# Performance work log

Measured on AMD Instinct MI355X. Metric: run time of the kernel, lower is better.

## Reference

```python
import jax, jax.numpy as jnp
import numpy as np

N, DIM_V, DIM_MM, DIM_O = 1024, 2048, 64, 2048
EPS_LOG = 1e-3


def setup_inputs() -> dict:
    key = jax.random.key(0)
    ks = jax.random.split(key, 12)
    feature_visual = jax.random.normal(ks[0], (N, DIM_V), dtype=jnp.float32)
    # valid boxes (x1, y1, x2, y2) inside an ~800x600 image
    x1 = jax.random.uniform(ks[1], (N, 1)) * 700.0
    y1 = jax.random.uniform(ks[2], (N, 1)) * 500.0
    w = jax.random.uniform(ks[3], (N, 1)) * 180.0 + 16.0
    h = jax.random.uniform(ks[4], (N, 1)) * 180.0 + 16.0
    rois = jnp.concatenate([x1, y1, x1 + w, y1 + h], axis=1)
    s = 0.02
    return {
        "feature_visual": feature_visual,
        "rois": rois,
        "Wk": jax.random.normal(ks[5], (DIM_V, DIM_MM), dtype=jnp.float32) * s,
        "bk": jnp.zeros((DIM_MM,), jnp.float32),
        "Wq": jax.random.normal(ks[6], (DIM_V, DIM_MM), dtype=jnp.float32) * s,
        "bq": jnp.zeros((DIM_MM,), jnp.float32),
        "Wv": jax.random.normal(ks[7], (DIM_V, DIM_O), dtype=jnp.float32) * s,
        "bv": jnp.zeros((DIM_O,), jnp.float32),
        "G1": jax.random.normal(ks[8], (4, DIM_MM), dtype=jnp.float32) * s,
        "g1": jnp.zeros((DIM_MM,), jnp.float32),
        "G2": jax.random.normal(ks[9], (DIM_MM, 1), dtype=jnp.float32) * s,
        "g2": jnp.zeros((1,), jnp.float32),
    }


def _geometry_weight(rois, G1, g1, G2, g2):
    # pairwise relative geometry features [N, N, 4], then MLP -> ReLU scalar weight [N, N]
    wh = rois[:, 2:4] - rois[:, 0:2]                      # [N, 2] box width/height
    ctr = 0.5 * (rois[:, 0:2] + rois[:, 2:4])             # [N, 2] centers
    d = ctr[None, :, :] - ctr[:, None, :]                 # [N, N, 2] (j relative to i)
    f12 = jnp.log(jnp.abs(d) / wh[:, None, :] + EPS_LOG)  # log(|dx|/wi), log(|dy|/hi)
    f34 = jnp.log(wh[None, :, :] / wh[:, None, :])        # log(wj/wi), log(hj/hi)
    geo = jnp.concatenate([f12, f34], axis=-1)            # [N, N, 4]
    h = jax.nn.relu(jnp.einsum('ijf,fm->ijm', geo, G1) + g1)
    w = jax.nn.relu(jnp.einsum('ijm,mo->ijo', h, G2) + g2)
    return w[..., 0]                                      # [N, N]


def reference(feature_visual, rois, Wk, bk, Wq, bq, Wv, bv, G1, g1, G2, g2):
    fv = jax.nn.relu(feature_visual)                      # pre-activation features
    k = fv @ Wk + bk                                      # [N, dim_mm]
    q = fv @ Wq + bq                                      # [N, dim_mm]
    v = fv @ Wv + bv                                      # [N, dim_o]
    scale = 1.0 / np.sqrt(DIM_MM).astype(np.float32)
    visual_weight = (q @ k.T) * scale                     # [N, N]: score[i,j] = <q_i... wait
    # torch: (query.unsqueeze(0) * key.unsqueeze(1)).sum(2) -> score[i,j] = <k_i, q_j>
    visual_weight = (k @ q.T) * scale
    geometry_weight = _geometry_weight(rois, G1, g1, G2, g2)
    attention = jnp.exp(visual_weight) * geometry_weight  # [N, N]
    n = attention.shape[0]
    attention = attention * (1.0 - jnp.eye(n, dtype=attention.dtype))  # zero diagonal
    attention = attention / (attention.sum(axis=1, keepdims=True) + 1e-10)
    return attention @ v                                  # [N, dim_o]
```

## Files before the change

kernel.cpp:

```cpp
#include <hip/hip_runtime.h>
#include <hip/hip_bf16.h>

#define NR 1024
#define DV 2048
#define DMM 64
#define DO 2048

typedef __attribute__((ext_vector_type(8))) __bf16 bf16x8;
typedef __attribute__((ext_vector_type(4))) float f32x4;

__device__ __forceinline__ float relu_f(float x) { return fmaxf(x, 0.f); }

__device__ __forceinline__ unsigned short f2bf(float x) {
    union { float f; unsigned int u; } v; v.f = x;
    unsigned int r = v.u + 0x7fffu + ((v.u >> 16) & 1u);
    return (unsigned short)(r >> 16);
}

__device__ __forceinline__ void gload_lds16(const void* g, void* l) {
    __builtin_amdgcn_global_load_lds(
        (const __attribute__((address_space(1))) void*)g,
        (__attribute__((address_space(3))) void*)l, 16, 0, 0);
}

__device__ __forceinline__ void transpose_tile(
    const float* __restrict__ W, unsigned short* __restrict__ Wt,
    int Ncols, int k0, int o0, float (*ld)[65])
{
    const int t = threadIdx.x;
    const int r = t >> 2;
    const int c0 = (t & 3) * 16;
    #pragma unroll
    for (int i = 0; i < 4; ++i) {
        float4 v = *reinterpret_cast<const float4*>(&W[(size_t)(k0 + r) * Ncols + o0 + c0 + i * 4]);
        ld[c0 + i * 4 + 0][r] = v.x;
        ld[c0 + i * 4 + 1][r] = v.y;
        ld[c0 + i * 4 + 2][r] = v.z;
        ld[c0 + i * 4 + 3][r] = v.w;
    }
    __syncthreads();
    const int o = t >> 2;
    const int kc = (t & 3) * 16;
    unsigned int u[8];
    #pragma unroll
    for (int j = 0; j < 8; ++j) {
        float x0 = ld[o][kc + 2 * j], x1 = ld[o][kc + 2 * j + 1];
        u[j] = (unsigned)f2bf(x0) | ((unsigned)f2bf(x1) << 16);
    }
    uint4* dst = reinterpret_cast<uint4*>(&Wt[(size_t)(o0 + o) * DV + k0 + kc]);
    dst[0] = make_uint4(u[0], u[1], u[2], u[3]);
    dst[1] = make_uint4(u[4], u[5], u[6], u[7]);
}

__global__ __launch_bounds__(256) void prep_kernel(
    const float* __restrict__ feat,
    const float* __restrict__ Wk, const float* __restrict__ Wq, const float* __restrict__ Wv,
    const float* __restrict__ rois,
    unsigned short* __restrict__ fvb, unsigned short* __restrict__ WkqT,
    unsigned short* __restrict__ WvT,
    float4* __restrict__ boxf, float2* __restrict__ boxinv)
{
    __shared__ float ld[64][65];
    const int bid = blockIdx.x;
    if (bid < 1024) {
        const int idx = bid * 256 + threadIdx.x;
        const float4 a = *reinterpret_cast<const float4*>(feat + (size_t)idx * 8);
        const float4 b = *reinterpret_cast<const float4*>(feat + (size_t)idx * 8 + 4);
        uint4 o;
        o.x = (unsigned)f2bf(relu_f(a.x)) | ((unsigned)f2bf(relu_f(a.y)) << 16);
        o.y = (unsigned)f2bf(relu_f(a.z)) | ((unsigned)f2bf(relu_f(a.w)) << 16);
        o.z = (unsigned)f2bf(relu_f(b.x)) | ((unsigned)f2bf(relu_f(b.y)) << 16);
        o.w = (unsigned)f2bf(relu_f(b.z)) | ((unsigned)f2bf(relu_f(b.w)) << 16);
        *reinterpret_cast<uint4*>(fvb + (size_t)idx * 8) = o;
    } else if (bid < 2048) {
        const int idx = bid - 1024;
        transpose_tile(Wv, WvT, DO, (idx >> 5) * 64, (idx & 31) * 64, ld);
    } else if (bid < 2080) {
        transpose_tile(Wk, WkqT, DMM, (bid - 2048) * 64, 0, ld);
    } else if (bid < 2112) {
        transpose_tile(Wq, WkqT + 64 * DV, DMM, (bid - 2080) * 64, 0, ld);
    } else {
        const int idx = (bid - 2112) * 256 + threadIdx.x;
        const float4 r = *reinterpret_cast<const float4*>(rois + (size_t)idx * 4);
        const float w = r.z - r.x, h = r.w - r.y;
        boxf[idx]   = make_float4(0.5f * (r.x + r.z), 0.5f * (r.y + r.w), __logf(w), __logf(h));
        boxinv[idx] = make_float2(1.f / w, 1.f / h);
    }
}

template<int NT, int LDA, int LDB>
__device__ __forceinline__ void mfma_tile_pipe(
    const unsigned short* __restrict__ A, const unsigned short* __restrict__ Bt,
    int bm0, int bn0, unsigned short* As, unsigned short* Bs, f32x4 (&acc)[2][4])
{
    const int t = threadIdx.x;
    const int w = t >> 6, lane = t & 63;
    const int wr = w >> 1, wc = w & 1;
    const int fr = lane & 15, fq = lane >> 4;
    const int sr = lane >> 3;
    const int sc = ((lane & 7) ^ sr) * 8;

    const unsigned short* ga0 = A  + (size_t)(bm0 + w * 16 +  0 + sr) * LDA + sc;
    const unsigned short* ga1 = A  + (size_t)(bm0 + w * 16 +  8 + sr) * LDA + sc;
    const unsigned short* gb0 = Bt + (size_t)(bn0 + w * 32 +  0 + sr) * LDB + sc;
    const unsigned short* gb1 = Bt + (size_t)(bn0 + w * 32 +  8 + sr) * LDB + sc;
    const unsigned short* gb2 = Bt + (size_t)(bn0 + w * 32 + 16 + sr) * LDB + sc;
    const unsigned short* gb3 = Bt + (size_t)(bn0 + w * 32 + 24 + sr) * LDB + sc;

#define STAGE(buf, ts_) do {                                                  \
        const size_t ko_ = (size_t)(ts_) * 64;                                \
        gload_lds16(ga0 + ko_, &As[(buf) * 4096 + w * 1024]);                 \
        gload_lds16(ga1 + ko_, &As[(buf) * 4096 + w * 1024 + 512]);           \
        gload_lds16(gb0 + ko_, &Bs[(buf) * 8192 + w * 2048]);                 \
        gload_lds16(gb1 + ko_, &Bs[(buf) * 8192 + w * 2048 + 512]);           \
        gload_lds16(gb2 + ko_, &Bs[(buf) * 8192 + w * 2048 + 1024]);          \
        gload_lds16(gb3 + ko_, &Bs[(buf) * 8192 + w * 2048 + 1536]);          \
    } while (0)

#define COMPUTE(buf) do {                                                                     \
        const int kx_ = fr & 7;                                                               \
        const int clo_ = (fq ^ kx_) * 8, chi_ = ((fq + 4) ^ kx_) * 8;                         \
        bf16x8 afl[2], afh[2], bfl[4], bfh[4];                                                \
        _Pragma("unroll")                                                                     \
        for (int m = 0; m < 2; ++m) {                                                         \
            const int rb = (buf) * 4096 + (wr * 32 + m * 16 + fr) * 64;                       \
            afl[m] = *reinterpret_cast<const bf16x8*>(&As[rb + clo_]);                        \
            afh[m] = *reinterpret_cast<const bf16x8*>(&As[rb + chi_]);                        \
        }                                                                                     \
        _Pragma("unroll")                                                                     \
        for (int n = 0; n < 4; ++n) {                                                         \
            const int cb = (buf) * 8192 + (wc * 64 + n * 16 + fr) * 64;                       \
            bfl[n] = *reinterpret_cast<const bf16x8*>(&Bs[cb + clo_]);                        \
            bfh[n] = *reinterpret_cast<const bf16x8*>(&Bs[cb + chi_]);                        \
        }                                                                                     \
        _Pragma("unroll")                                                                     \
        for (int m = 0; m < 2; ++m)                                                           \
            _Pragma("unroll")                                                                 \
            for (int n = 0; n < 4; ++n) {                                                     \
                acc[m][n] = __builtin_amdgcn_mfma_f32_16x16x32_bf16(afl[m], bfl[n], acc[m][n], 0, 0, 0); \
                acc[m][n] = __builtin_amdgcn_mfma_f32_16x16x32_bf16(afh[m], bfh[n], acc[m][n], 0, 0, 0); \
            }                                                                                 \
    } while (0)

    STAGE(0, 0);
    if (NT > 1) STAGE(1, 1);

    #pragma unroll 2
    for (int ts = 0; ts < NT - 1; ++ts) {
        asm volatile("s_waitcnt vmcnt(6)" ::: "memory");
        asm volatile("s_barrier" ::: "memory");
        COMPUTE(ts & 1);
        asm volatile("s_barrier" ::: "memory");
        if (ts + 2 < NT) STAGE(ts & 1, ts + 2);
    }
    asm volatile("s_waitcnt vmcnt(0)" ::: "memory");
    asm volatile("s_barrier" ::: "memory");
    COMPUTE((NT - 1) & 1);
#undef STAGE
#undef COMPUTE
}

__global__ __launch_bounds__(256) void gemm_vt_kq(
    const unsigned short* __restrict__ WvT, const unsigned short* __restrict__ fvb,
    const unsigned short* __restrict__ WkqT,
    const float* __restrict__ bv, const float* __restrict__ bk, const float* __restrict__ bq,
    unsigned short* __restrict__ vT, unsigned short* __restrict__ kqb)
{
    __shared__ unsigned short As[2 * 64 * 64];
    __shared__ unsigned short Bs[2 * 128 * 64];
    const int bid = blockIdx.x;
    const bool is_kq = bid >= 256;
    const unsigned short* A  = is_kq ? fvb  : WvT;
    const unsigned short* Bt = is_kq ? WkqT : fvb;
    const int bm0 = is_kq ? (bid - 256) * 64 : (bid >> 3) * 64;
    const int bn0 = is_kq ? 0 : (bid & 7) * 128;

    f32x4 acc[2][4] = {};
    mfma_tile_pipe<DV / 64, DV, DV>(A, Bt, bm0, bn0, As, Bs, acc);

    const int t = threadIdx.x;
    const int w = t >> 6, lane = t & 63;
    const int wr = w >> 1, wc = w & 1;
    const int fr = lane & 15, fq = lane >> 4;
    if (!is_kq) {
        #pragma unroll
        for (int m = 0; m < 2; ++m)
            #pragma unroll
            for (int r = 0; r < 4; ++r) {
                const int row = bm0 + wr * 32 + m * 16 + fq * 4 + r;
                const float badd = bv[row];
                #pragma unroll
                for (int n = 0; n < 4; ++n) {
                    const int col = bn0 + wc * 64 + n * 16 + fr;
                    vT[(size_t)row * NR + col] = f2bf(acc[m][n][r] + badd);
                }
            }
    } else {
        #pragma unroll
        for (int m = 0; m < 2; ++m)
            #pragma unroll
            for (int r = 0; r < 4; ++r) {
                const int row = bm0 + wr * 32 + m * 16 + fq * 4 + r;
                #pragma unroll
                for (int n = 0; n < 4; ++n) {
                    const int col = wc * 64 + n * 16 + fr;
                    const float badd = (col < 64) ? bk[col] : bq[col - 64];
                    kqb[(size_t)row * 128 + col] = f2bf(acc[m][n][r] + badd);
                }
            }
    }
}

__global__ __launch_bounds__(256) void gemm_s(
    const unsigned short* __restrict__ kqb, float* __restrict__ S)
{
    __shared__ unsigned short As[2 * 64 * 64];
    __shared__ unsigned short Bs[2 * 128 * 64];
    const int bm0 = blockIdx.y * 64;
    const int bn0 = blockIdx.x * 128;
    f32x4 acc[2][4] = {};
    mfma_tile_pipe<1, 128, 128>(kqb, kqb + 64, bm0, bn0, As, Bs, acc);
    const int t = threadIdx.x;
    const int w = t >> 6, lane = t & 63;
    const int wr = w >> 1, wc = w & 1;
    const int fr = lane & 15, fq = lane >> 4;
    #pragma unroll
    for (int m = 0; m < 2; ++m)
        #pragma unroll
        for (int r = 0; r < 4; ++r) {
            const int row = bm0 + wr * 32 + m * 16 + fq * 4 + r;
            #pragma unroll
            for (int n = 0; n < 4; ++n) {
                const int col = bn0 + wc * 64 + n * 16 + fr;
                S[(size_t)row * NR + col] = acc[m][n][r] * 0.125f;
            }
        }
}

__global__ __launch_bounds__(256) void gemm_out(
    const unsigned short* __restrict__ attb, const unsigned short* __restrict__ vT,
    float* __restrict__ out)
{
    __shared__ unsigned short As[2 * 64 * 64];
    __shared__ unsigned short Bs[2 * 128 * 64];
    const int bm0 = blockIdx.y * 64;
    const int bn0 = blockIdx.x * 128;
    f32x4 acc[2][4] = {};
    mfma_tile_pipe<NR / 64, NR, NR>(attb, vT, bm0, bn0, As, Bs, acc);
    const int t = threadIdx.x;
    const int w = t >> 6, lane = t & 63;
    const int wr = w >> 1, wc = w & 1;
    const int fr = lane & 15, fq = lane >> 4;
    #pragma unroll
    for (int m = 0; m < 2; ++m)
        #pragma unroll
        for (int r = 0; r < 4; ++r) {
            const int row = bm0 + wr * 32 + m * 16 + fq * 4 + r;
            #pragma unroll
            for (int n = 0; n < 4; ++n) {
                const int col = bn0 + wc * 64 + n * 16 + fr;
                out[(size_t)row * DO + col] = acc[m][n][r];
            }
        }
}

#define MLP_STEP(A_, B_, C_, D_, E_, F_)                                            \
    {                                                                               \
        float h_ = fmaf(ff1[ch], A_, fmaf(ff2[ch], B_, fmaf(ff3[ch], C_,            \
                   fmaf(ff4[ch], D_, E_))));                                        \
        h_ = fmaxf(h_, 0.f);                                                        \
        gw[ch] = fmaf(h_, F_, gw[ch]);                                              \
    }

__global__ __launch_bounds__(256) void attn_kernel(
    const float* __restrict__ S,
    const float4* __restrict__ boxf, const float2* __restrict__ boxinv,
    const float* __restrict__ G1, const float* __restrict__ g1,
    const float* __restrict__ G2, const float* __restrict__ g2,
    unsigned short* __restrict__ att)
{
    __shared__ float G1s[4][64];
    __shared__ float g1s[64];
    __shared__ float G2s[64];
    __shared__ float red[4];
    const int i = blockIdx.x;
    const int t = threadIdx.x;
    if (t < 64) {
        G1s[0][t] = G1[t];
        G1s[1][t] = G1[64 + t];
        G1s[2][t] = G1[128 + t];
        G1s[3][t] = G1[192 + t];
        g1s[t] = g1[t];
        G2s[t] = G2[t];
    }
    __syncthreads();
    const float4 bi = boxf[i];
    const float2 ivi = boxinv[i];
    const float g2v = g2[0];

    float ff1[4], ff2[4], ff3[4], ff4[4], sc[4], gw[4] = {0.f, 0.f, 0.f, 0.f};
    #pragma unroll
    for (int ch = 0; ch < 4; ++ch) {
        const int j = ch * 256 + t;
        const float4 bj = boxf[j];
        sc[ch] = S[(size_t)i * NR + j];
        ff1[ch] = __logf(fmaf(fabsf(bj.x - bi.x), ivi.x, 1e-3f));
        ff2[ch] = __logf(fmaf(fabsf(bj.y - bi.y), ivi.y, 1e-3f));
        ff3[ch] = bj.z - bi.z;
        ff4[ch] = bj.w - bi.w;
    }

    for (int mt = 0; mt < 64; mt += 8) {
        const float4 A0 = *reinterpret_cast<const float4*>(&G1s[0][mt]);
        const float4 A1 = *reinterpret_cast<const float4*>(&G1s[0][mt + 4]);
        const float4 B0 = *reinterpret_cast<const float4*>(&G1s[1][mt]);
        const float4 B1 = *reinterpret_cast<const float4*>(&G1s[1][mt + 4]);
        const float4 C0 = *reinterpret_cast<const float4*>(&G1s[2][mt]);
        const float4 C1 = *reinterpret_cast<const float4*>(&G1s[2][mt + 4]);
        const float4 D0 = *reinterpret_cast<const float4*>(&G1s[3][mt]);
        const float4 D1 = *reinterpret_cast<const float4*>(&G1s[3][mt + 4]);
        const float4 E0 = *reinterpret_cast<const float4*>(&g1s[mt]);
        const float4 E1 = *reinterpret_cast<const float4*>(&g1s[mt + 4]);
        const float4 F0 = *reinterpret_cast<const float4*>(&G2s[mt]);
        const float4 F1 = *reinterpret_cast<const float4*>(&G2s[mt + 4]);
        #pragma unroll
        for (int ch = 0; ch < 4; ++ch) {
            MLP_STEP(A0.x, B0.x, C0.x, D0.x, E0.x, F0.x)
            MLP_STEP(A0.y, B0.y, C0.y, D0.y, E0.y, F0.y)
            MLP_STEP(A0.z, B0.z, C0.z, D0.z, E0.z, F0.z)
            MLP_STEP(A0.w, B0.w, C0.w, D0.w, E0.w, F0.w)
            MLP_STEP(A1.x, B1.x, C1.x, D1.x, E1.x, F1.x)
            MLP_STEP(A1.y, B1.y, C1.y, D1.y, E1.y, F1.y)
            MLP_STEP(A1.z, B1.z, C1.z, D1.z, E1.z, F1.z)
            MLP_STEP(A1.w, B1.w, C1.w, D1.w, E1.w, F1.w)
        }
    }

    float vals[4];
    float rsum = 0.f;
    #pragma unroll
    for (int ch = 0; ch < 4; ++ch) {
        const float gwp = fmaxf(gw[ch] + g2v, 0.f);
        float a = __expf(sc[ch]) * gwp;
        if (ch * 256 + t == i) a = 0.f;
        vals[ch] = a;
        rsum += a;
    }
    #pragma unroll
    for (int o = 32; o > 0; o >>= 1) rsum += __shfl_down(rsum, o, 64);
    if ((t & 63) == 0) red[t >> 6] = rsum;
    __syncthreads();
    const float inv = 1.f / (red[0] + red[1] + red[2] + red[3] + 1e-10f);
    #pragma unroll
    for (int ch = 0; ch < 4; ++ch)
        att[(size_t)i * NR + ch * 256 + t] = f2bf(vals[ch] * inv);
}

extern "C" void kernel_launch(void* const* d_in, const int* in_sizes, int n_in,
                              void* d_out, int out_size, void* d_ws, size_t ws_size,
                              hipStream_t stream) {
    const float* feat = (const float*)d_in[0];
    const float* rois = (const float*)d_in[1];
    const float* Wk   = (const float*)d_in[2];
    const float* bk   = (const float*)d_in[3];
    const float* Wq   = (const float*)d_in[4];
    const float* bq   = (const float*)d_in[5];
    const float* Wv   = (const float*)d_in[6];
    const float* bv   = (const float*)d_in[7];
    const float* G1   = (const float*)d_in[8];
    const float* g1   = (const float*)d_in[9];
    const float* G2   = (const float*)d_in[10];
    const float* g2   = (const float*)d_in[11];
    float* out = (float*)d_out;
    char* ws = (char*)d_ws;

    unsigned short* kqb  = (unsigned short*)ws;
    float4* boxf         = (float4*)(ws + (256 << 10));
    float2* boxinv       = (float2*)(ws + (272 << 10));
    unsigned short* fvb  = (unsigned short*)(ws + (512 << 10));
    unsigned short* WvT  = (unsigned short*)(ws + (512 << 10) + (4 << 20));
    unsigned short* WkqT = (unsigned short*)(ws + (512 << 10) + (12 << 20));
    unsigned short* vT   = (unsigned short*)(ws + (1024 << 10) + (12 << 20));
    unsigned short* attb = (unsigned short*)(ws + (1024 << 10) + (16 << 20));
    float* Sbuf          = (float*)(ws + (1024 << 10) + (18 << 20));

    prep_kernel<<<2116, 256, 0, stream>>>(feat, Wk, Wq, Wv, rois, fvb, WkqT, WvT, boxf, boxinv);
    gemm_vt_kq<<<272, 256, 0, stream>>>(WvT, fvb, WkqT, bv, bk, bq, vT, kqb);
    gemm_s<<<dim3(8, 16), 256, 0, stream>>>(kqb, Sbuf);
    attn_kernel<<<NR, 256, 0, stream>>>(Sbuf, boxf, boxinv, G1, g1, G2, g2, attb);
    gemm_out<<<dim3(DO / 128, NR / 64), 256, 0, stream>>>(attb, vT, out);
}
```

Measured before the change: 64.77 us.

## Fuse score GEMM into attention kernel with per-row bf16 dot products

Removes the separate k·qᵀ MFMA GEMM kernel and its fp32 score buffer; each attention block now computes its row of scores directly from the bf16 k/q buffer with scalar FMAs. This avoids one launch and the write and read-back of the N×N score matrix. In exchange the attention kernel does extra ALU work and issues strided 16-byte loads of q rows that depend on L2 reuse.

```diff
diff --git a/kernel.cpp b/kernel.cpp
--- a/kernel.cpp
+++ b/kernel.cpp
@@ -15,6 +15,13 @@
     union { float f; unsigned int u; } v; v.f = x;
     unsigned int r = v.u + 0x7fffu + ((v.u >> 16) & 1u);
     return (unsigned short)(r >> 16);
+}
+
+__device__ __forceinline__ float bflo(unsigned int u) {
+    union { unsigned int x; float f; } v; v.x = u << 16; return v.f;
+}
+__device__ __forceinline__ float bfhi(unsigned int u) {
+    union { unsigned int x; float f; } v; v.x = u & 0xffff0000u; return v.f;
 }
 
 __device__ __forceinline__ void gload_lds16(const void* g, void* l) {
@@ -211,32 +218,6 @@
     }
 }
 
-__global__ __launch_bounds__(256) void gemm_s(
-    const unsigned short* __restrict__ kqb, float* __restrict__ S)
-{
-    __shared__ unsigned short As[2 * 64 * 64];
-    __shared__ unsigned short Bs[2 * 128 * 64];
-    const int bm0 = blockIdx.y * 64;
-    const int bn0 = blockIdx.x * 128;
-    f32x4 acc[2][4] = {};
-    mfma_tile_pipe<1, 128, 128>(kqb, kqb + 64, bm0, bn0, As, Bs, acc);
-    const int t = threadIdx.x;
-    const int w = t >> 6, lane = t & 63;
-    const int wr = w >> 1, wc = w & 1;
-    const int fr = lane & 15, fq = lane >> 4;
-    #pragma unroll
-    for (int m = 0; m < 2; ++m)
-        #pragma unroll
-        for (int r = 0; r < 4; ++r) {
-            const int row = bm0 + wr * 32 + m * 16 + fq * 4 + r;
-            #pragma unroll
-            for (int n = 0; n < 4; ++n) {
-                const int col = bn0 + wc * 64 + n * 16 + fr;
-                S[(size_t)row * NR + col] = acc[m][n][r] * 0.125f;
-            }
-        }
-}
-
 __global__ __launch_bounds__(256) void gemm_out(
     const unsigned short* __restrict__ attb, const unsigned short* __restrict__ vT,
     float* __restrict__ out)
@@ -273,7 +254,7 @@
     }
 
 __global__ __launch_bounds__(256) void attn_kernel(
-    const float* __restrict__ S,
+    const unsigned short* __restrict__ kqb,
     const float4* __restrict__ boxf, const float2* __restrict__ boxinv,
     const float* __restrict__ G1, const float* __restrict__ g1,
     const float* __restrict__ G2, const float* __restrict__ g2,
@@ -282,6 +263,7 @@
     __shared__ float G1s[4][64];
     __shared__ float g1s[64];
     __shared__ float G2s[64];
+    __shared__ float ksf[64];
     __shared__ float red[4];
     const int i = blockIdx.x;
     const int t = threadIdx.x;
@@ -292,18 +274,38 @@
         G1s[3][t] = G1[192 + t];
         g1s[t] = g1[t];
         G2s[t] = G2[t];
+        ksf[t] = bflo((unsigned int)kqb[(size_t)i * 128 + t]);
     }
     __syncthreads();
     const float4 bi = boxf[i];
     const float2 ivi = boxinv[i];
     const float g2v = g2[0];
 
+    float dot[4] = {0.f, 0.f, 0.f, 0.f};
+    #pragma unroll
+    for (int c4 = 0; c4 < 8; ++c4) {
+        const float4 k0 = *reinterpret_cast<const float4*>(&ksf[c4 * 8]);
+        const float4 k1 = *reinterpret_cast<const float4*>(&ksf[c4 * 8 + 4]);
+        #pragma unroll
+        for (int ch = 0; ch < 4; ++ch) {
+            const int j = ch * 256 + t;
+            const uint4 qv = *reinterpret_cast<const uint4*>(
+                &kqb[(size_t)j * 128 + 64 + c4 * 8]);
+            float d = dot[ch];
+            d = fmaf(k0.x, bflo(qv.x), d); d = fmaf(k0.y, bfhi(qv.x), d);
+            d = fmaf(k0.z, bflo(qv.y), d); d = fmaf(k0.w, bfhi(qv.y), d);
+            d = fmaf(k1.x, bflo(qv.z), d); d = fmaf(k1.y, bfhi(qv.z), d);
+            d = fmaf(k1.z, bflo(qv.w), d); d = fmaf(k1.w, bfhi(qv.w), d);
+            dot[ch] = d;
+        }
+    }
+
     float ff1[4], ff2[4], ff3[4], ff4[4], sc[4], gw[4] = {0.f, 0.f, 0.f, 0.f};
     #pragma unroll
     for (int ch = 0; ch < 4; ++ch) {
         const int j = ch * 256 + t;
         const float4 bj = boxf[j];
-        sc[ch] = S[(size_t)i * NR + j];
+        sc[ch] = dot[ch] * 0.125f;
         ff1[ch] = __logf(fmaf(fabsf(bj.x - bi.x), ivi.x, 1e-3f));
         ff2[ch] = __logf(fmaf(fabsf(bj.y - bi.y), ivi.y, 1e-3f));
         ff3[ch] = bj.z - bi.z;
@@ -382,11 +384,9 @@
     unsigned short* WkqT = (unsigned short*)(ws + (512 << 10) + (12 << 20));
     unsigned short* vT   = (unsigned short*)(ws + (1024 << 10) + (12 << 20));
     unsigned short* attb = (unsigned short*)(ws + (1024 << 10) + (16 << 20));
-    float* Sbuf          = (float*)(ws + (1024 << 10) + (18 << 20));
 
     prep_kernel<<<2116, 256, 0, stream>>>(feat, Wk, Wq, Wv, rois, fvb, WkqT, WvT, boxf, boxinv);
     gemm_vt_kq<<<272, 256, 0, stream>>>(WvT, fvb, WkqT, bv, bk, bq, vT, kqb);
-    gemm_s<<<dim3(8, 16), 256, 0, stream>>>(kqb, Sbuf);
-    attn_kernel<<<NR, 256, 0, stream>>>(Sbuf, boxf, boxinv, G1, g1, G2, g2, attb);
+    attn_kernel<<<NR, 256, 0, stream>>>(kqb, boxf, boxinv, G1, g1, G2, g2, attb);
     gemm_out<<<dim3(DO / 128, NR / 64), 256, 0, stream>>>(attb, vT, out);
 }
```

After: 84.64 us. +30.7%, slower.

## Fuse score GEMM with geometry MLP and defer row normalization into output GEMM

Applied to the files above, without the earlier changes.

Merges the S=k·qᵀ GEMM and the geometry/attention kernel into a single tiled kernel. The geometry MLP now runs directly on the MFMA accumulator fragments, so the fp32 S buffer is no longer written and read back. Row-sum normalization moves into the final attention·V GEMM, which sums the bf16 A tiles while it loads them and scales the output rows. This removes one launch and a 4 MB intermediate round trip. In exchange it adds per-element box loads in the fused kernel and normalizes with sums of bf16-rounded values instead of fp32 values.

```diff
diff --git a/kernel.cpp b/kernel.cpp
--- a/kernel.cpp
+++ b/kernel.cpp
@@ -7,6 +7,7 @@
 #define DO 2048
 
 typedef __attribute__((ext_vector_type(8))) __bf16 bf16x8;
+typedef __attribute__((ext_vector_type(8))) unsigned short u16x8;
 typedef __attribute__((ext_vector_type(4))) float f32x4;
 
 __device__ __forceinline__ float relu_f(float x) { return fmaxf(x, 0.f); }
@@ -15,6 +16,10 @@
     union { float f; unsigned int u; } v; v.f = x;
     unsigned int r = v.u + 0x7fffu + ((v.u >> 16) & 1u);
     return (unsigned short)(r >> 16);
+}
+
+__device__ __forceinline__ float bflo(unsigned int u) {
+    union { unsigned int x; float f; } v; v.x = u << 16; return v.f;
 }
 
 __device__ __forceinline__ void gload_lds16(const void* g, void* l) {
@@ -88,10 +93,11 @@
     }
 }
 
-template<int NT, int LDA, int LDB>
+template<int NT, int LDA, int LDB, int BNR, bool SUMA>
 __device__ __forceinline__ void mfma_tile_pipe(
     const unsigned short* __restrict__ A, const unsigned short* __restrict__ Bt,
-    int bm0, int bn0, unsigned short* As, unsigned short* Bs, f32x4 (&acc)[2][4])
+    int bm0, int bn0, unsigned short* As, unsigned short* Bs,
+    f32x4 (&acc)[2][BNR], float* rs)
 {
     const int t = threadIdx.x;
     const int w = t >> 6, lane = t & 63;
@@ -100,27 +106,27 @@
     const int sr = lane >> 3;
     const int sc = ((lane & 7) ^ sr) * 8;
 
-    const unsigned short* ga0 = A  + (size_t)(bm0 + w * 16 +  0 + sr) * LDA + sc;
-    const unsigned short* ga1 = A  + (size_t)(bm0 + w * 16 +  8 + sr) * LDA + sc;
-    const unsigned short* gb0 = Bt + (size_t)(bn0 + w * 32 +  0 + sr) * LDB + sc;
-    const unsigned short* gb1 = Bt + (size_t)(bn0 + w * 32 +  8 + sr) * LDB + sc;
-    const unsigned short* gb2 = Bt + (size_t)(bn0 + w * 32 + 16 + sr) * LDB + sc;
-    const unsigned short* gb3 = Bt + (size_t)(bn0 + w * 32 + 24 + sr) * LDB + sc;
-
-#define STAGE(buf, ts_) do {                                                  \
-        const size_t ko_ = (size_t)(ts_) * 64;                                \
-        gload_lds16(ga0 + ko_, &As[(buf) * 4096 + w * 1024]);                 \
-        gload_lds16(ga1 + ko_, &As[(buf) * 4096 + w * 1024 + 512]);           \
-        gload_lds16(gb0 + ko_, &Bs[(buf) * 8192 + w * 2048]);                 \
-        gload_lds16(gb1 + ko_, &Bs[(buf) * 8192 + w * 2048 + 512]);           \
-        gload_lds16(gb2 + ko_, &Bs[(buf) * 8192 + w * 2048 + 1024]);          \
-        gload_lds16(gb3 + ko_, &Bs[(buf) * 8192 + w * 2048 + 1536]);          \
+    const unsigned short* ga0 = A + (size_t)(bm0 + w * 16 + 0 + sr) * LDA + sc;
+    const unsigned short* ga1 = A + (size_t)(bm0 + w * 16 + 8 + sr) * LDA + sc;
+    const unsigned short* gb[BNR];
+    #pragma unroll
+    for (int g = 0; g < BNR; ++g)
+        gb[g] = Bt + (size_t)(bn0 + w * (BNR * 8) + g * 8 + sr) * LDB + sc;
+
+#define STAGE(buf, ts_) do {                                                   \
+        const size_t ko_ = (size_t)(ts_) * 64;                                 \
+        gload_lds16(ga0 + ko_, &As[(buf) * 4096 + w * 1024]);                  \
+        gload_lds16(ga1 + ko_, &As[(buf) * 4096 + w * 1024 + 512]);            \
+        _Pragma("unroll")                                                      \
+        for (int g = 0; g < BNR; ++g)                                          \
+            gload_lds16(gb[g] + ko_,                                           \
+                &Bs[(buf) * (BNR * 2048) + w * (BNR * 512) + g * 512]);        \
     } while (0)
 
 #define COMPUTE(buf) do {                                                                     \
         const int kx_ = fr & 7;                                                               \
         const int clo_ = (fq ^ kx_) * 8, chi_ = ((fq + 4) ^ kx_) * 8;                         \
-        bf16x8 afl[2], afh[2], bfl[4], bfh[4];                                                \
+        bf16x8 afl[2], afh[2], bfl[BNR], bfh[BNR];                                            \
         _Pragma("unroll")                                                                     \
         for (int m = 0; m < 2; ++m) {                                                         \
             const int rb = (buf) * 4096 + (wr * 32 + m * 16 + fr) * 64;                       \
@@ -128,15 +134,25 @@
             afh[m] = *reinterpret_cast<const bf16x8*>(&As[rb + chi_]);                        \
         }                                                                                     \
         _Pragma("unroll")                                                                     \
-        for (int n = 0; n < 4; ++n) {                                                         \
-            const int cb = (buf) * 8192 + (wc * 64 + n * 16 + fr) * 64;                       \
+        for (int n = 0; n < BNR; ++n) {                                                       \
+            const int cb = (buf) * (BNR * 2048) + (wc * (BNR * 16) + n * 16 + fr) * 64;       \
             bfl[n] = *reinterpret_cast<const bf16x8*>(&Bs[cb + clo_]);                        \
             bfh[n] = *reinterpret_cast<const bf16x8*>(&Bs[cb + chi_]);                        \
+        }                                                                                     \
+        if (SUMA && wc == 0) {                                                                \
+            _Pragma("unroll")                                                                 \
+            for (int m = 0; m < 2; ++m) {                                                     \
+                u16x8 sl = __builtin_bit_cast(u16x8, afl[m]);                                 \
+                u16x8 sh = __builtin_bit_cast(u16x8, afh[m]);                                 \
+                _Pragma("unroll")                                                             \
+                for (int e = 0; e < 8; ++e)                                                   \
+                    rs[m] += bflo(sl[e]) + bflo(sh[e]);                                       \
+            }                                                                                 \
         }                                                                                     \
         _Pragma("unroll")                                                                     \
         for (int m = 0; m < 2; ++m)                                                           \
             _Pragma("unroll")                                                                 \
-            for (int n = 0; n < 4; ++n) {                                                     \
+            for (int n = 0; n < BNR; ++n) {                                                   \
                 acc[m][n] = __builtin_amdgcn_mfma_f32_16x16x32_bf16(afl[m], bfl[n], acc[m][n], 0, 0, 0); \
                 acc[m][n] = __builtin_amdgcn_mfma_f32_16x16x32_bf16(afh[m], bfh[n], acc[m][n], 0, 0, 0); \
             }                                                                                 \
@@ -147,7 +163,8 @@
 
     #pragma unroll 2
     for (int ts = 0; ts < NT - 1; ++ts) {
-        asm volatile("s_waitcnt vmcnt(6)" ::: "memory");
+        if (BNR == 4) { asm volatile("s_waitcnt vmcnt(6)" ::: "memory"); }
+        else          { asm volatile("s_waitcnt vmcnt(4)" ::: "memory"); }
         asm volatile("s_barrier" ::: "memory");
         COMPUTE(ts & 1);
         asm volatile("s_barrier" ::: "memory");
@@ -176,7 +193,7 @@
     const int bn0 = is_kq ? 0 : (bid & 7) * 128;
 
     f32x4 acc[2][4] = {};
-    mfma_tile_pipe<DV / 64, DV, DV>(A, Bt, bm0, bn0, As, Bs, acc);
+    mfma_tile_pipe<DV / 64, DV, DV, 4, false>(A, Bt, bm0, bn0, As, Bs, acc, nullptr);
 
     const int t = threadIdx.x;
     const int w = t >> 6, lane = t & 63;
@@ -211,79 +228,29 @@
     }
 }
 
-__global__ __launch_bounds__(256) void gemm_s(
-    const unsigned short* __restrict__ kqb, float* __restrict__ S)
-{
-    __shared__ unsigned short As[2 * 64 * 64];
-    __shared__ unsigned short Bs[2 * 128 * 64];
-    const int bm0 = blockIdx.y * 64;
-    const int bn0 = blockIdx.x * 128;
-    f32x4 acc[2][4] = {};
-    mfma_tile_pipe<1, 128, 128>(kqb, kqb + 64, bm0, bn0, As, Bs, acc);
-    const int t = threadIdx.x;
-    const int w = t >> 6, lane = t & 63;
-    const int wr = w >> 1, wc = w & 1;
-    const int fr = lane & 15, fq = lane >> 4;
-    #pragma unroll
-    for (int m = 0; m < 2; ++m)
-        #pragma unroll
-        for (int r = 0; r < 4; ++r) {
-            const int row = bm0 + wr * 32 + m * 16 + fq * 4 + r;
-            #pragma unroll
-            for (int n = 0; n < 4; ++n) {
-                const int col = bn0 + wc * 64 + n * 16 + fr;
-                S[(size_t)row * NR + col] = acc[m][n][r] * 0.125f;
-            }
-        }
-}
-
-__global__ __launch_bounds__(256) void gemm_out(
-    const unsigned short* __restrict__ attb, const unsigned short* __restrict__ vT,
-    float* __restrict__ out)
-{
-    __shared__ unsigned short As[2 * 64 * 64];
-    __shared__ unsigned short Bs[2 * 128 * 64];
-    const int bm0 = blockIdx.y * 64;
-    const int bn0 = blockIdx.x * 128;
-    f32x4 acc[2][4] = {};
-    mfma_tile_pipe<NR / 64, NR, NR>(attb, vT, bm0, bn0, As, Bs, acc);
-    const int t = threadIdx.x;
-    const int w = t >> 6, lane = t & 63;
-    const int wr = w >> 1, wc = w & 1;
-    const int fr = lane & 15, fq = lane >> 4;
-    #pragma unroll
-    for (int m = 0; m < 2; ++m)
-        #pragma unroll
-        for (int r = 0; r < 4; ++r) {
-            const int row = bm0 + wr * 32 + m * 16 + fq * 4 + r;
-            #pragma unroll
-            for (int n = 0; n < 4; ++n) {
-                const int col = bn0 + wc * 64 + n * 16 + fr;
-                out[(size_t)row * DO + col] = acc[m][n][r];
-            }
-        }
-}
-
-#define MLP_STEP(A_, B_, C_, D_, E_, F_)                                            \
+#define MLP_STEP8(A_, B_, C_, D_, E_, F_)                                           \
     {                                                                               \
-        float h_ = fmaf(ff1[ch], A_, fmaf(ff2[ch], B_, fmaf(ff3[ch], C_,            \
-                   fmaf(ff4[ch], D_, E_))));                                        \
-        h_ = fmaxf(h_, 0.f);                                                        \
-        gw[ch] = fmaf(h_, F_, gw[ch]);                                              \
-    }
-
-__global__ __launch_bounds__(256) void attn_kernel(
-    const float* __restrict__ S,
+        _Pragma("unroll")                                                           \
+        for (int p = 0; p < 8; ++p) {                                               \
+            float h_ = fmaf(ff1[p], A_, fmaf(ff2[p], B_, fmaf(ff3[p], C_,           \
+                       fmaf(ff4[p], D_, E_))));                                     \
+            h_ = fmaxf(h_, 0.f);                                                    \
+            gw[p] = fmaf(h_, F_, gw[p]);                                            \
+        }                                                                           \
+    }
+
+__global__ __launch_bounds__(256) void s_geo(
+    const unsigned short* __restrict__ kqb,
     const float4* __restrict__ boxf, const float2* __restrict__ boxinv,
     const float* __restrict__ G1, const float* __restrict__ g1,
     const float* __restrict__ G2, const float* __restrict__ g2,
     unsigned short* __restrict__ att)
 {
+    __shared__ unsigned short As[64 * 64];
+    __shared__ unsigned short Bs[64 * 64];
     __shared__ float G1s[4][64];
     __shared__ float g1s[64];
     __shared__ float G2s[64];
-    __shared__ float red[4];
-    const int i = blockIdx.x;
     const int t = threadIdx.x;
     if (t < 64) {
         G1s[0][t] = G1[t];
@@ -294,66 +261,118 @@
         G2s[t] = G2[t];
     }
     __syncthreads();
-    const float4 bi = boxf[i];
-    const float2 ivi = boxinv[i];
+
+    const int bm0 = blockIdx.y * 64;
+    const int bn0 = blockIdx.x * 64;
+    f32x4 acc[2][2] = {};
+    mfma_tile_pipe<1, 128, 128, 2, false>(kqb, kqb + 64, bm0, bn0, As, Bs, acc, nullptr);
+
+    const int w = t >> 6, lane = t & 63;
+    const int wr = w >> 1, wc = w & 1;
+    const int fr = lane & 15, fq = lane >> 4;
     const float g2v = g2[0];
 
-    float ff1[4], ff2[4], ff3[4], ff4[4], sc[4], gw[4] = {0.f, 0.f, 0.f, 0.f};
     #pragma unroll
-    for (int ch = 0; ch < 4; ++ch) {
-        const int j = ch * 256 + t;
-        const float4 bj = boxf[j];
-        sc[ch] = S[(size_t)i * NR + j];
-        ff1[ch] = __logf(fmaf(fabsf(bj.x - bi.x), ivi.x, 1e-3f));
-        ff2[ch] = __logf(fmaf(fabsf(bj.y - bi.y), ivi.y, 1e-3f));
-        ff3[ch] = bj.z - bi.z;
-        ff4[ch] = bj.w - bi.w;
-    }
-
-    for (int mt = 0; mt < 64; mt += 8) {
-        const float4 A0 = *reinterpret_cast<const float4*>(&G1s[0][mt]);
-        const float4 A1 = *reinterpret_cast<const float4*>(&G1s[0][mt + 4]);
-        const float4 B0 = *reinterpret_cast<const float4*>(&G1s[1][mt]);
-        const float4 B1 = *reinterpret_cast<const float4*>(&G1s[1][mt + 4]);
-        const float4 C0 = *reinterpret_cast<const float4*>(&G1s[2][mt]);
-        const float4 C1 = *reinterpret_cast<const float4*>(&G1s[2][mt + 4]);
-        const float4 D0 = *reinterpret_cast<const float4*>(&G1s[3][mt]);
-        const float4 D1 = *reinterpret_cast<const float4*>(&G1s[3][mt + 4]);
-        const float4 E0 = *reinterpret_cast<const float4*>(&g1s[mt]);
-        const float4 E1 = *reinterpret_cast<const float4*>(&g1s[mt + 4]);
-        const float4 F0 = *reinterpret_cast<const float4*>(&G2s[mt]);
-        const float4 F1 = *reinterpret_cast<const float4*>(&G2s[mt + 4]);
-        #pragma unroll
-        for (int ch = 0; ch < 4; ++ch) {
-            MLP_STEP(A0.x, B0.x, C0.x, D0.x, E0.x, F0.x)
-            MLP_STEP(A0.y, B0.y, C0.y, D0.y, E0.y, F0.y)
-            MLP_STEP(A0.z, B0.z, C0.z, D0.z, E0.z, F0.z)
-            MLP_STEP(A0.w, B0.w, C0.w, D0.w, E0.w, F0.w)
-            MLP_STEP(A1.x, B1.x, C1.x, D1.x, E1.x, F1.x)
-            MLP_STEP(A1.y, B1.y, C1.y, D1.y, E1.y, F1.y)
-            MLP_STEP(A1.z, B1.z, C1.z, D1.z, E1.z, F1.z)
-            MLP_STEP(A1.w, B1.w, C1.w, D1.w, E1.w, F1.w)
+    for (int m = 0; m < 2; ++m) {
+        const int rbase = bm0 + wr * 32 + m * 16 + fq * 4;
+        float ff1[8], ff2[8], ff3[8], ff4[8], sv[8], gw[8];
+        #pragma unroll
+        for (int n = 0; n < 2; ++n) {
+            const int col = bn0 + wc * 32 + n * 16 + fr;
+            const float4 bj = boxf[col];
+            #pragma unroll
+            for (int r = 0; r < 4; ++r) {
+                const int row = rbase + r;
+                const float4 bi = boxf[row];
+                const float2 ivi = boxinv[row];
+                const int p = n * 4 + r;
+                sv[p] = acc[m][n][r] * 0.125f;
+                ff1[p] = __logf(fmaf(fabsf(bj.x - bi.x), ivi.x, 1e-3f));
+                ff2[p] = __logf(fmaf(fabsf(bj.y - bi.y), ivi.y, 1e-3f));
+                ff3[p] = bj.z - bi.z;
+                ff4[p] = bj.w - bi.w;
+                gw[p] = 0.f;
+            }
         }
-    }
-
-    float vals[4];
-    float rsum = 0.f;
+        for (int mt = 0; mt < 64; mt += 8) {
+            const float4 A0 = *reinterpret_cast<const float4*>(&G1s[0][mt]);
+            const float4 A1 = *reinterpret_cast<const float4*>(&G1s[0][mt + 4]);
+            const float4 B0 = *reinterpret_cast<const float4*>(&G1s[1][mt]);
+            const float4 B1 = *reinterpret_cast<const float4*>(&G1s[1][mt + 4]);
+            const float4 C0 = *reinterpret_cast<const float4*>(&G1s[2][mt]);
+            const float4 C1 = *reinterpret_cast<const float4*>(&G1s[2][mt + 4]);
+            const float4 D0 = *reinterpret_cast<const float4*>(&G1s[3][mt]);
+            const float4 D1 = *reinterpret_cast<const float4*>(&G1s[3][mt + 4]);
+            const float4 E0 = *reinterpret_cast<const float4*>(&g1s[mt]);
+            const float4 E1 = *reinterpret_cast<const float4*>(&g1s[mt + 4]);
+            const float4 F0 = *reinterpret_cast<const float4*>(&G2s[mt]);
+            const float4 F1 = *reinterpret_cast<const float4*>(&G2s[mt + 4]);
+            MLP_STEP8(A0.x, B0.x, C0.x, D0.x, E0.x, F0.x)
+            MLP_STEP8(A0.y, B0.y, C0.y, D0.y, E0.y, F0.y)
+            MLP_STEP8(A0.z, B0.z, C0.z, D0.z, E0.z, F0.z)
+            MLP_STEP8(A0.w, B0.w, C0.w, D0.w, E0.w, F0.w)
+            MLP_STEP8(A1.x, B1.x, C1.x, D1.x, E1.x, F1.x)
+            MLP_STEP8(A1.y, B1.y, C1.y, D1.y, E1.y, F1.y)
+            MLP_STEP8(A1.z, B1.z, C1.z, D1.z, E1.z, F1.z)
+            MLP_STEP8(A1.w, B1.w, C1.w, D1.w, E1.w, F1.w)
+        }
+        #pragma unroll
+        for (int n = 0; n < 2; ++n) {
+            const int col = bn0 + wc * 32 + n * 16 + fr;
+            #pragma unroll
+            for (int r = 0; r < 4; ++r) {
+                const int row = rbase + r;
+                const int p = n * 4 + r;
+                float a = __expf(sv[p]) * fmaxf(gw[p] + g2v, 0.f);
+                if (row == col) a = 0.f;
+                att[(size_t)row * NR + col] = f2bf(a);
+            }
+        }
+    }
+}
+
+__global__ __launch_bounds__(256) void gemm_out(
+    const unsigned short* __restrict__ attb, const unsigned short* __restrict__ vT,
+    float* __restrict__ out)
+{
+    __shared__ unsigned short As[2 * 64 * 64];
+    __shared__ unsigned short Bs[2 * 128 * 64];
+    __shared__ float sinv[64];
+    const int bm0 = blockIdx.y * 64;
+    const int bn0 = blockIdx.x * 128;
+    f32x4 acc[2][4] = {};
+    float rs[2] = {0.f, 0.f};
+    mfma_tile_pipe<NR / 64, NR, NR, 4, true>(attb, vT, bm0, bn0, As, Bs, acc, rs);
+
+    const int t = threadIdx.x;
+    const int w = t >> 6, lane = t & 63;
+    const int wr = w >> 1, wc = w & 1;
+    const int fr = lane & 15, fq = lane >> 4;
+
+    if (wc == 0) {
+        #pragma unroll
+        for (int m = 0; m < 2; ++m) {
+            float v = rs[m];
+            v += __shfl_xor(v, 16, 64);
+            v += __shfl_xor(v, 32, 64);
+            if (fq == 0) sinv[wr * 32 + m * 16 + fr] = 1.0f / (v + 1e-10f);
+        }
+    }
+    __syncthreads();
+
     #pragma unroll
-    for (int ch = 0; ch < 4; ++ch) {
-        const float gwp = fmaxf(gw[ch] + g2v, 0.f);
-        float a = __expf(sc[ch]) * gwp;
-        if (ch * 256 + t == i) a = 0.f;
-        vals[ch] = a;
-        rsum += a;
-    }
-    #pragma unroll
-    for (int o = 32; o > 0; o >>= 1) rsum += __shfl_down(rsum, o, 64);
-    if ((t & 63) == 0) red[t >> 6] = rsum;
-    __syncthreads();
-    const float inv = 1.f / (red[0] + red[1] + red[2] + red[3] + 1e-10f);
-    #pragma unroll
-    for (int ch = 0; ch < 4; ++ch)
-        att[(size_t)i * NR + ch * 256 + t] = f2bf(vals[ch] * inv);
+    for (int m = 0; m < 2; ++m)
+        #pragma unroll
+        for (int r = 0; r < 4; ++r) {
+            const int rl = wr * 32 + m * 16 + fq * 4 + r;
+            const int row = bm0 + rl;
+            const float sc_ = sinv[rl];
+            #pragma unroll
+            for (int n = 0; n < 4; ++n) {
+                const int col = bn0 + wc * 64 + n * 16 + fr;
+                out[(size_t)row * DO + col] = acc[m][n][r] * sc_;
+            }
+        }
 }
 
 extern "C" void kernel_launch(void* const* d_in, const int* in_sizes, int n_in,
@@ -382,11 +401,9 @@
     unsigned short* WkqT = (unsigned short*)(ws + (512 << 10) + (12 << 20));
     unsigned short* vT   = (unsigned short*)(ws + (1024 << 10) + (12 << 20));
     unsigned short* attb = (unsigned short*)(ws + (1024 << 10) + (16 << 20));
-    float* Sbuf          = (float*)(ws + (1024 << 10) + (18 << 20));
 
     prep_kernel<<<2116, 256, 0, stream>>>(feat, Wk, Wq, Wv, rois, fvb, WkqT, WvT, boxf, boxinv);
     gemm_vt_kq<<<272, 256, 0, stream>>>(WvT, fvb, WkqT, bv, bk, bq, vT, kqb);
-    gemm_s<<<dim3(8, 16), 256, 0, stream>>>(kqb, Sbuf);
-    attn_kernel<<<NR, 256, 0, stream>>>(Sbuf, boxf, boxinv, G1, g1, G2, g2, attb);
+    s_geo<<<dim3(16, 16), 256, 0, stream>>>(kqb, boxf, boxinv, G1, g1, G2, g2, attb);
     gemm_out<<<dim3(DO / 128, NR / 64), 256, 0, stream>>>(attb, vT, out);
 }
```

Result: slower. 68.22 us (+5.3%).
